# Performance work log

Measured on AMD Instinct MI355X. Metric: run time of the kernel, lower is better.

## Reference

```python
import jax, jax.numpy as jnp
import numpy as np

B = 32; D = 192; DEPTH = 4; DI = 384; DS = 16; DC = 4; P = 16; IMG = 224; N = 196; NC = 2


def setup_inputs() -> dict:
    key = jax.random.key(0)
    ks = iter(jax.random.split(key, 20))
    rn = lambda shape, s=0.02: jax.random.normal(next(ks), shape, dtype=jnp.float32) * s
    inp = {}
    inp["x"] = jax.random.normal(next(ks), (B, 3, IMG, IMG), dtype=jnp.float32)
    inp["patch_w"] = rn((D, 3 * P * P)); inp["patch_b"] = jnp.zeros((D,), jnp.float32)
    inp["cls_token"] = rn((1, 1, D)); inp["pos_embed"] = rn((1, N + 1, D))
    inp["ln_g"] = jnp.ones((DEPTH, D), jnp.float32); inp["ln_b"] = jnp.zeros((DEPTH, D), jnp.float32)
    inp["w_in"] = rn((DEPTH, 2 * DI, D))
    inp["conv_w"] = rn((DEPTH, DI, DC)); inp["conv_b"] = jnp.zeros((DEPTH, DI), jnp.float32)
    inp["w_x"] = rn((DEPTH, 2 * DS + 1, DI))
    inp["w_dt"] = rn((DEPTH, DI)); inp["b_dt"] = jnp.zeros((DEPTH, DI), jnp.float32)
    A = jnp.tile(jnp.arange(1, DS + 1, dtype=jnp.float32)[None, None, :], (DEPTH, DI, 1))
    inp["A_log"] = jnp.log(A)
    inp["D_ssm"] = jnp.ones((DEPTH, DI), jnp.float32)
    inp["w_out"] = rn((DEPTH, D, DI))
    inp["fn_g"] = jnp.ones((D,), jnp.float32); inp["fn_b"] = jnp.zeros((D,), jnp.float32)
    inp["cls_w"] = rn((NC, D)); inp["cls_b"] = jnp.zeros((NC,), jnp.float32)
    inp["reg_w1"] = rn((D // 2, D)); inp["reg_b1"] = jnp.zeros((D // 2,), jnp.float32)
    inp["reg_w2"] = rn((1, D // 2)); inp["reg_b2"] = jnp.zeros((1,), jnp.float32)
    return inp


def _ln(x, g, b):
    m = x.mean(-1, keepdims=True)
    v = ((x - m) ** 2).mean(-1, keepdims=True)
    return (x - m) / jnp.sqrt(v + 1e-5) * g + b


def _mamba(x, w_in, conv_w, conv_b, w_x, w_dt, b_dt, A_log, D_ssm, w_out):
    Bb, L, _ = x.shape
    xz = jnp.einsum('bld,ed->ble', x, w_in)           # [B,L,2*DI]
    xc, z = xz[..., :DI], xz[..., DI:]
    # causal depthwise conv1d (torch pads both sides then slices [:L] -> left-pad DC-1)
    xct = jnp.transpose(xc, (0, 2, 1))                 # [B,DI,L]
    xpad = jnp.pad(xct, ((0, 0), (0, 0), (DC - 1, 0)))
    conv = sum(conv_w[:, k, None] * xpad[:, :, k:k + L] for k in range(DC)) + conv_b[:, None]
    xa = jax.nn.silu(jnp.transpose(conv, (0, 2, 1)))   # [B,L,DI]
    bcd = jnp.einsum('bld,nd->bln', xa, w_x)           # [B,L,2*DS+1]
    Bm = bcd[..., :DS]; Cm = bcd[..., DS:2 * DS]
    dt = jax.nn.softplus(bcd[..., -1:] * w_dt + b_dt)  # [B,L,DI]  (Linear(1,DI))
    A = -jnp.exp(A_log)                                # [DI,DS]
    dA = jnp.exp(dt[..., None] * A)                    # [B,L,DI,DS]
    dBx = dt[..., None] * Bm[:, :, None, :] * xa[..., None]

    def step(h, inp):
        dA_t, dBx_t, C_t = inp
        h = dA_t * h + dBx_t
        return h, jnp.einsum('bdn,bn->bd', h, C_t)

    h0 = jnp.zeros((Bb, DI, DS), dtype=x.dtype)
    _, ys = jax.lax.scan(step, h0, (dA.transpose(1, 0, 2, 3), dBx.transpose(1, 0, 2, 3), Cm.transpose(1, 0, 2)))
    y = jnp.transpose(ys, (1, 0, 2)) + xa * D_ssm
    return jnp.einsum('bli,di->bld', y * jax.nn.silu(z), w_out)


def reference(x, patch_w, patch_b, cls_token, pos_embed, ln_g, ln_b, w_in, conv_w, conv_b,
              w_x, w_dt, b_dt, A_log, D_ssm, w_out, fn_g, fn_b, cls_w, cls_b,
              reg_w1, reg_b1, reg_w2, reg_b2):
    Bb = x.shape[0]
    H = IMG // P
    # non-overlapping patchify == Conv2d(kernel=stride=P)
    patches = x.reshape(Bb, 3, H, P, H, P).transpose(0, 2, 4, 1, 3, 5).reshape(Bb, N, 3 * P * P)
    tok = patches @ patch_w.T + patch_b
    t = jnp.concatenate([jnp.broadcast_to(cls_token, (Bb, 1, D)), tok], axis=1) + pos_embed
    for i in range(DEPTH):
        t = t + _mamba(_ln(t, ln_g[i], ln_b[i]), w_in[i], conv_w[i], conv_b[i],
                       w_x[i], w_dt[i], b_dt[i], A_log[i], D_ssm[i], w_out[i])
    feat = _ln(t, fn_g, fn_b)[:, 0]
    cls = feat @ cls_w.T + cls_b
    reg = jax.nn.gelu(feat @ reg_w1.T + reg_b1, approximate=False) @ reg_w2.T + reg_b2
    return (cls, reg)
```

## Files before the change

kernel.cpp:

```cpp
#include <hip/hip_runtime.h>
#include <hip/hip_bf16.h>
#include <math.h>

#define B_ 32
#define D_ 192
#define DEPTH_ 4
#define DI_ 384
#define DS_ 16
#define DC_ 4
#define P_ 16
#define IMG_ 224
#define N_ 196
#define L_ 197

#define NCH 16
#define CHL 13

typedef short s16x8 __attribute__((ext_vector_type(8)));
typedef float f32x16 __attribute__((ext_vector_type(16)));

__device__ __forceinline__ float sigmoidf_(float x) { return 1.f / (1.f + expf(-x)); }

__global__ __launch_bounds__(256) void k_prep(const float* __restrict__ patch_w,
                                              const float* __restrict__ w_in,
                                              const float* __restrict__ w_out,
                                              const float* __restrict__ w_x,
                                              const float* __restrict__ cls_tok,
                                              const float* __restrict__ pos,
                                              const float* __restrict__ A_log,
                                              __hip_bfloat16* __restrict__ pw,
                                              __hip_bfloat16* __restrict__ win,
                                              __hip_bfloat16* __restrict__ wout,
                                              __hip_bfloat16* __restrict__ wx,
                                              float* __restrict__ t,
                                              float* __restrict__ Aneg) {
  int idx = blockIdx.x * 256 + threadIdx.x;
  if (idx < 147456) { pw[idx] = __float2bfloat16(patch_w[idx]); return; }
  idx -= 147456;
  if (idx < 589824) { win[idx] = __float2bfloat16(w_in[idx]); return; }
  idx -= 589824;
  if (idx < 294912) { wout[idx] = __float2bfloat16(w_out[idx]); return; }
  idx -= 294912;
  if (idx < 98304) {
    int li = idx / 24576;
    int r = (idx / 384) & 63;
    int c = idx % 384;
    wx[idx] = (r < 33) ? __float2bfloat16(w_x[(li * 33 + r) * 384 + c]) : __float2bfloat16(0.f);
    return;
  }
  idx -= 98304;
  if (idx < 6144) {
    int b = idx / 192, d = idx % 192;
    t[(size_t)b * L_ * D_ + d] = cls_tok[d] + pos[d];
    return;
  }
  idx -= 6144;
  Aneg[idx] = -expf(A_log[idx]);
}

__global__ __launch_bounds__(256) void k_im2col(const float* __restrict__ x,
                                                __hip_bfloat16* __restrict__ A) {
  int idx = blockIdx.x * 256 + threadIdx.x;
  int tok = idx / 768, f = idx - tok * 768;
  int b = tok / 196, p = tok - b * 196;
  int h = p / 14, w = p - h * 14;
  int c = f >> 8, i = (f >> 4) & 15, j = f & 15;
  float v = x[(((size_t)(b * 3 + c) * 224 + h * 16 + i) * 224 + w * 16 + j)];
  A[idx] = __float2bfloat16(v);
}

template <int KTOT, int MODE>
__global__ __launch_bounds__(256) void k_gemm_mfma(const short* __restrict__ A,
                                                   const short* __restrict__ Wb,
                                                   float* __restrict__ C,
                                                   const float* __restrict__ bias,
                                                   const float* __restrict__ pos,
                                                   int M) {
  constexpr int KC = 96;
  constexpr int STR = 104;
  __shared__ __align__(16) short Als[64 * STR];
  __shared__ __align__(16) short Bls[64 * STR];
  int m0 = blockIdx.x * 64, n0 = blockIdx.y * 64;
  int tid = threadIdx.x;
  int lane = tid & 63, wid = tid >> 6;
  int mw = (wid & 1) * 32, nw = (wid >> 1) * 32;
  int l31 = lane & 31, lh = lane >> 5;
  f32x16 acc;
#pragma unroll
  for (int i = 0; i < 16; i++) acc[i] = 0.f;
  for (int kc = 0; kc < KTOT; kc += KC) {
    __syncthreads();
#pragma unroll
    for (int i = 0; i < 3; i++) {
      int seg = tid + i * 256;
      int r = seg / 12, s = seg - r * 12;
      *(s16x8*)(Als + r * STR + s * 8) =
          *(const s16x8*)(A + (size_t)(m0 + r) * KTOT + kc + s * 8);
      *(s16x8*)(Bls + r * STR + s * 8) =
          *(const s16x8*)(Wb + (size_t)(n0 + r) * KTOT + kc + s * 8);
    }
    __syncthreads();
#pragma unroll
    for (int ks = 0; ks < KC / 16; ks++) {
      s16x8 af = *(const s16x8*)(Als + (mw + l31) * STR + ks * 16 + lh * 8);
      s16x8 bf = *(const s16x8*)(Bls + (nw + l31) * STR + ks * 16 + lh * 8);
      acc = __builtin_amdgcn_mfma_f32_32x32x16_bf16(af, bf, acc, 0, 0, 0);
    }
  }
  int gn = n0 + nw + l31;
#pragma unroll
  for (int i = 0; i < 16; i++) {
    int rowt = mw + (i & 3) + 8 * (i >> 2) + 4 * lh;
    int gm = m0 + rowt;
    float v = acc[i];
    if (MODE == 1) {
      if (gm < M) C[(size_t)gm * 192 + gn] += v;
    } else if (MODE == 3) {
      if (gm < M) C[(size_t)gm * 64 + gn] = v;
    } else if (MODE == 4) {
      if (gm < M) ((__hip_bfloat16*)C)[(size_t)gm * 768 + gn] = __float2bfloat16(v);
    } else {
      int b = gm / 196, p = gm - b * 196;
      C[((size_t)b * 197 + 1 + p) * 192 + gn] =
          v + bias[gn] + pos[(size_t)(1 + p) * 192 + gn];
    }
  }
}

__global__ __launch_bounds__(256) void k_ln_bf(const float* __restrict__ t,
                                               const float* __restrict__ g,
                                               const float* __restrict__ bb,
                                               __hip_bfloat16* __restrict__ o) {
  int tok = blockIdx.x * 4 + (threadIdx.x >> 6);
  int tid = threadIdx.x & 63;
  const float* xr = t + (size_t)tok * D_;
  float x0 = xr[tid], x1 = xr[tid + 64], x2 = xr[tid + 128];
  float s = x0 + x1 + x2;
  float q = x0 * x0 + x1 * x1 + x2 * x2;
#pragma unroll
  for (int off = 1; off < 64; off <<= 1) {
    s += __shfl_xor(s, off, 64);
    q += __shfl_xor(q, off, 64);
  }
  float m = s * (1.f / 192.f);
  float r = rsqrtf(q * (1.f / 192.f) - m * m + 1e-5f);
  __hip_bfloat16* orow = o + (size_t)tok * D_;
  orow[tid]       = __float2bfloat16((x0 - m) * r * g[tid]       + bb[tid]);
  orow[tid + 64]  = __float2bfloat16((x1 - m) * r * g[tid + 64]  + bb[tid + 64]);
  orow[tid + 128] = __float2bfloat16((x2 - m) * r * g[tid + 128] + bb[tid + 128]);
}

__global__ __launch_bounds__(384) void k_conv(const __hip_bfloat16* __restrict__ xz,
                                              const float* __restrict__ cw_,
                                              const float* __restrict__ cb,
                                              __hip_bfloat16* __restrict__ xa_bf,
                                              __hip_bfloat16* __restrict__ sz_bf) {
  __shared__ float xs[11][384];
  int r0 = blockIdx.x * 8;
  int d = threadIdx.x;
#pragma unroll
  for (int row = 0; row < 11; row++) {
    int gr = r0 - 3 + row;
    if (gr >= 0) xs[row][d] = __bfloat162float(xz[(size_t)gr * 768 + d]);
  }
  __syncthreads();
  float4 cw = *(const float4*)(cw_ + d * 4);
  float cbv = cb[d];
#pragma unroll
  for (int tk = 0; tk < 8; tk++) {
    int tok = r0 + tk;
    int l = tok % L_;
    float acc = fmaf(cw.w, xs[tk + 3][d], cbv);
    if (l >= 1) acc = fmaf(cw.z, xs[tk + 2][d], acc);
    if (l >= 2) acc = fmaf(cw.y, xs[tk + 1][d], acc);
    if (l >= 3) acc = fmaf(cw.x, xs[tk][d], acc);
    float xav = acc * sigmoidf_(acc);
    xa_bf[(size_t)tok * DI_ + d] = __float2bfloat16(xav);
    float z = __bfloat162float(xz[(size_t)tok * 768 + 384 + d]);
    sz_bf[(size_t)tok * DI_ + d] = __float2bfloat16(z * sigmoidf_(z));
  }
}

__global__ __launch_bounds__(384) void k_scan1(const __hip_bfloat16* __restrict__ xa,
                                               const float* __restrict__ bcd,
                                               const float* __restrict__ Aneg,
                                               const float* __restrict__ w_dt,
                                               const float* __restrict__ b_dt,
                                               float* __restrict__ Pst,
                                               float* __restrict__ Hst) {
  int b = blockIdx.x >> 4, ch = blockIdx.x & 15;
  int d = threadIdx.x;
  int l0 = ch * CHL;
  int lim = min(CHL, L_ - l0);
  float Av[16];
#pragma unroll
  for (int q = 0; q < 4; q++) {
    float4 v = *(const float4*)(Aneg + d * 16 + q * 4);
    Av[q * 4] = v.x; Av[q * 4 + 1] = v.y; Av[q * 4 + 2] = v.z; Av[q * 4 + 3] = v.w;
  }
  float wdt = w_dt[d], bdt = b_dt[d];
  const __hip_bfloat16* xap = xa + ((size_t)b * L_ + l0) * DI_ + d;
  const float* bp = bcd + ((size_t)b * L_ + l0) * 64;
  float h[16], Pp[16];
#pragma unroll
  for (int n = 0; n < 16; n++) { h[n] = 0.f; Pp[n] = 1.f; }
  float xv = __bfloat162float(xap[0]);
  for (int j = 0; j < lim; j++) {
    int jn = (j + 1 < lim) ? (j + 1) : j;
    float xn = __bfloat162float(xap[(size_t)jn * DI_]);
    float dtraw = bp[j * 64 + 32];
    float Bn[16];
#pragma unroll
    for (int n = 0; n < 16; n++) Bn[n] = bp[j * 64 + n];
    float v = fmaf(dtraw, wdt, bdt);
    float dtv = (v > 20.f) ? v : __logf(1.f + __expf(v));
    float dtx = dtv * xv;
#pragma unroll
    for (int n = 0; n < 16; n++) {
      float dA = __expf(dtv * Av[n]);
      h[n] = fmaf(dA, h[n], dtx * Bn[n]);
      Pp[n] *= dA;
    }
    xv = xn;
  }
  size_t s = ((size_t)blockIdx.x * 384 + d) * 16;
#pragma unroll
  for (int q = 0; q < 4; q++) {
    *(float4*)(Pst + s + q * 4) = make_float4(Pp[q * 4], Pp[q * 4 + 1], Pp[q * 4 + 2], Pp[q * 4 + 3]);
    *(float4*)(Hst + s + q * 4) = make_float4(h[q * 4], h[q * 4 + 1], h[q * 4 + 2], h[q * 4 + 3]);
  }
}

__global__ __launch_bounds__(256) void k_scan_mid(const float* __restrict__ Pst,
                                                  const float* __restrict__ Hst,
                                                  float* __restrict__ Hinit) {
  int idx = blockIdx.x * 256 + threadIdx.x;
  int b = idx / 6144, r = idx - b * 6144;
  float h = 0.f;
#pragma unroll
  for (int c = 0; c < NCH; c++) {
    size_t o = (size_t)(b * NCH + c) * 6144 + r;
    Hinit[o] = h;
    h = fmaf(Pst[o], h, Hst[o]);
  }
}

__global__ __launch_bounds__(384) void k_scan2(const __hip_bfloat16* __restrict__ xa,
                                               const __hip_bfloat16* __restrict__ sz,
                                               const float* __restrict__ bcd,
                                               const float* __restrict__ Aneg,
                                               const float* __restrict__ D_ssm,
                                               const float* __restrict__ w_dt,
                                               const float* __restrict__ b_dt,
                                               const float* __restrict__ Hinit,
                                               __hip_bfloat16* __restrict__ y) {
  int b = blockIdx.x >> 4, ch = blockIdx.x & 15;
  int d = threadIdx.x;
  int l0 = ch * CHL;
  int lim = min(CHL, L_ - l0);
  float Av[16];
#pragma unroll
  for (int q = 0; q < 4; q++) {
    float4 v = *(const float4*)(Aneg + d * 16 + q * 4);
    Av[q * 4] = v.x; Av[q * 4 + 1] = v.y; Av[q * 4 + 2] = v.z; Av[q * 4 + 3] = v.w;
  }
  float Dv = D_ssm[d];
  float wdt = w_dt[d], bdt = b_dt[d];
  const __hip_bfloat16* xap = xa + ((size_t)b * L_ + l0) * DI_ + d;
  const __hip_bfloat16* szp = sz + ((size_t)b * L_ + l0) * DI_ + d;
  const float* bp = bcd + ((size_t)b * L_ + l0) * 64;
  __hip_bfloat16* yp = y + ((size_t)b * L_ + l0) * DI_ + d;
  float h[16];
  {
    size_t s = ((size_t)blockIdx.x * 384 + d) * 16;
#pragma unroll
    for (int q = 0; q < 4; q++) {
      float4 v = *(const float4*)(Hinit + s + q * 4);
      h[q * 4] = v.x; h[q * 4 + 1] = v.y; h[q * 4 + 2] = v.z; h[q * 4 + 3] = v.w;
    }
  }
  float xv = __bfloat162float(xap[0]);
  float szv = __bfloat162float(szp[0]);
  for (int j = 0; j < lim; j++) {
    int jn = (j + 1 < lim) ? (j + 1) : j;
    float xn = __bfloat162float(xap[(size_t)jn * DI_]);
    float szn = __bfloat162float(szp[(size_t)jn * DI_]);
    float dtraw = bp[j * 64 + 32];
    float Bn[16], Cn[16];
#pragma unroll
    for (int n = 0; n < 16; n++) Bn[n] = bp[j * 64 + n];
#pragma unroll
    for (int n = 0; n < 16; n++) Cn[n] = bp[j * 64 + 16 + n];
    float v = fmaf(dtraw, wdt, bdt);
    float dtv = (v > 20.f) ? v : __logf(1.f + __expf(v));
    float dtx = dtv * xv;
    float acc = 0.f;
#pragma unroll
    for (int n = 0; n < 16; n++) {
      float dA = __expf(dtv * Av[n]);
      h[n] = fmaf(dA, h[n], dtx * Bn[n]);
      acc = fmaf(h[n], Cn[n], acc);
    }
    float yv = fmaf(xv, Dv, acc) * szv;
    yp[(size_t)j * DI_] = __float2bfloat16(yv);
    xv = xn; szv = szn;
  }
}

__global__ __launch_bounds__(192) void k_head(const float* __restrict__ t,
                                              const float* __restrict__ fn_g,
                                              const float* __restrict__ fn_b,
                                              const float* __restrict__ cls_w,
                                              const float* __restrict__ cls_b,
                                              const float* __restrict__ rw1,
                                              const float* __restrict__ rb1,
                                              const float* __restrict__ rw2,
                                              const float* __restrict__ rb2,
                                              float* __restrict__ out) {
  __shared__ float red[8];
  __shared__ float stats[2];
  __shared__ float feat_s[192];
  __shared__ float h_s[96];
  int b = blockIdx.x, tid = threadIdx.x;
  float x = t[(size_t)b * L_ * D_ + tid];
  float s = x, q = x * x;
#pragma unroll
  for (int off = 1; off < 64; off <<= 1) {
    s += __shfl_xor(s, off, 64);
    q += __shfl_xor(q, off, 64);
  }
  int w = tid >> 6;
  if ((tid & 63) == 0) { red[w] = s; red[4 + w] = q; }
  __syncthreads();
  if (tid == 0) {
    float ss = red[0] + red[1] + red[2];
    float qq = red[4] + red[5] + red[6];
    float m = ss * (1.f / 192.f);
    stats[0] = m;
    stats[1] = rsqrtf(qq * (1.f / 192.f) - m * m + 1e-5f);
  }
  __syncthreads();
  float fv = (x - stats[0]) * stats[1] * fn_g[tid] + fn_b[tid];
  feat_s[tid] = fv;
  __syncthreads();
  if (tid < 96) {
    float a = rb1[tid];
    const float* wr = rw1 + (size_t)tid * 192;
    for (int k = 0; k < 192; k++) a = fmaf(feat_s[k], wr[k], a);
    h_s[tid] = 0.5f * a * (1.f + erff(a * 0.70710678118654752f));
  } else if (tid < 98) {
    int c = tid - 96;
    float a = cls_b[c];
    const float* wr = cls_w + (size_t)c * 192;
    for (int k = 0; k < 192; k++) a = fmaf(feat_s[k], wr[k], a);
    out[b * 2 + c] = a;
  }
  __syncthreads();
  if (tid == 0) {
    float a = rb2[0];
    for (int j = 0; j < 96; j++) a = fmaf(h_s[j], rw2[j], a);
    out[64 + b] = a;
  }
}

extern "C" void kernel_launch(void* const* d_in, const int* in_sizes, int n_in,
                              void* d_out, int out_size, void* d_ws, size_t ws_size,
                              hipStream_t stream) {
  const float* x       = (const float*)d_in[0];
  const float* patch_w = (const float*)d_in[1];
  const float* patch_b = (const float*)d_in[2];
  const float* cls_tok = (const float*)d_in[3];
  const float* pos     = (const float*)d_in[4];
  const float* ln_g    = (const float*)d_in[5];
  const float* ln_b    = (const float*)d_in[6];
  const float* w_in    = (const float*)d_in[7];
  const float* conv_w  = (const float*)d_in[8];
  const float* conv_b  = (const float*)d_in[9];
  const float* w_x     = (const float*)d_in[10];
  const float* w_dt    = (const float*)d_in[11];
  const float* b_dt    = (const float*)d_in[12];
  const float* A_log   = (const float*)d_in[13];
  const float* D_ssm   = (const float*)d_in[14];
  const float* w_out   = (const float*)d_in[15];
  const float* fn_g    = (const float*)d_in[16];
  const float* fn_b    = (const float*)d_in[17];
  const float* cls_w   = (const float*)d_in[18];
  const float* cls_b   = (const float*)d_in[19];
  const float* reg_w1  = (const float*)d_in[20];
  const float* reg_b1  = (const float*)d_in[21];
  const float* reg_w2  = (const float*)d_in[22];
  const float* reg_b2  = (const float*)d_in[23];
  float* out = (float*)d_out;

  float* ws = (float*)d_ws;
  float* t_buf = ws;
  float* bcd   = t_buf + 1210368;
  float* Pst   = bcd + 405504;
  float* Hst   = Pst + 3145728;
  float* Hinit = Hst + 3145728;
  float* Aneg  = Hinit + 3145728;
  __hip_bfloat16* xz_bf  = (__hip_bfloat16*)(Aneg + 24576);
  __hip_bfloat16* Abuf   = xz_bf;
  __hip_bfloat16* xa_bf  = xz_bf + 4841472;
  __hip_bfloat16* sz_bf  = xa_bf + 2433024;
  __hip_bfloat16* xln_bf = sz_bf + 2433024;
  __hip_bfloat16* y_bf   = xln_bf + 1216512;
  __hip_bfloat16* pw_bf  = y_bf + 2433024;
  __hip_bfloat16* win_bf = pw_bf + 147456;
  __hip_bfloat16* wout_bf = win_bf + 589824;
  __hip_bfloat16* wx_bf  = wout_bf + 294912;

  k_prep<<<4536, 256, 0, stream>>>(patch_w, w_in, w_out, w_x, cls_tok, pos, A_log,
                                   pw_bf, win_bf, wout_bf, wx_bf, t_buf, Aneg);
  k_im2col<<<18816, 256, 0, stream>>>(x, Abuf);
  k_gemm_mfma<768, 2><<<dim3(98, 3), 256, 0, stream>>>(
      (const short*)Abuf, (const short*)pw_bf, t_buf, patch_b, pos, 6272);

  for (int i = 0; i < DEPTH_; i++) {
    k_ln_bf<<<1576, 256, 0, stream>>>(t_buf, ln_g + i * D_, ln_b + i * D_, xln_bf);
    k_gemm_mfma<192, 4><<<dim3(99, 12), 256, 0, stream>>>(
        (const short*)xln_bf, (const short*)(win_bf + (size_t)i * 147456), (float*)xz_bf,
        nullptr, nullptr, 6304);
    k_conv<<<788, 384, 0, stream>>>(xz_bf, conv_w + i * DI_ * DC_, conv_b + i * DI_,
                                    xa_bf, sz_bf);
    k_gemm_mfma<384, 3><<<dim3(99, 1), 256, 0, stream>>>(
        (const short*)xa_bf, (const short*)(wx_bf + (size_t)i * 24576), bcd,
        nullptr, nullptr, 6304);
    k_scan1<<<B_ * NCH, 384, 0, stream>>>(xa_bf, bcd, Aneg + i * 6144,
                                          w_dt + i * DI_, b_dt + i * DI_, Pst, Hst);
    k_scan_mid<<<768, 256, 0, stream>>>(Pst, Hst, Hinit);
    k_scan2<<<B_ * NCH, 384, 0, stream>>>(xa_bf, sz_bf, bcd, Aneg + i * 6144,
                                          D_ssm + i * DI_, w_dt + i * DI_, b_dt + i * DI_,
                                          Hinit, y_bf);
    k_gemm_mfma<384, 1><<<dim3(99, 3), 256, 0, stream>>>(
        (const short*)y_bf, (const short*)(wout_bf + (size_t)i * 73728), t_buf,
        nullptr, nullptr, 6304);
  }
  k_head<<<32, 192, 0, stream>>>(t_buf, fn_g, fn_b, cls_w, cls_b, reg_w1, reg_b1,
                                 reg_w2, reg_b2, out);
}
```

Before: 462.0 us.

## Fuse LayerNorm into in-projection GEMM, fold scan carry into scan2, merge prep

LayerNorm is now computed inside the in-projection GEMM prologue, so the normalized bf16 activations never go through global memory and one launch per layer is removed. The separate inter-chunk scan kernel is dropped, and each scan2 block instead serially combines the preceding chunks' P/H states itself. The weight-prep and im2col kernels are merged into one launch. The cost is redundant work: LN is recomputed for every N tile (12x), and later chunks in scan2 read up to 15 chunk states each.

```diff
diff --git a/kernel.cpp b/kernel.cpp
--- a/kernel.cpp
+++ b/kernel.cpp
@@ -17,24 +17,35 @@
 #define CHL 13
 
 typedef short s16x8 __attribute__((ext_vector_type(8)));
+typedef short s16x4 __attribute__((ext_vector_type(4)));
 typedef float f32x16 __attribute__((ext_vector_type(16)));
 
 __device__ __forceinline__ float sigmoidf_(float x) { return 1.f / (1.f + expf(-x)); }
-
-__global__ __launch_bounds__(256) void k_prep(const float* __restrict__ patch_w,
-                                              const float* __restrict__ w_in,
-                                              const float* __restrict__ w_out,
-                                              const float* __restrict__ w_x,
-                                              const float* __restrict__ cls_tok,
-                                              const float* __restrict__ pos,
-                                              const float* __restrict__ A_log,
-                                              __hip_bfloat16* __restrict__ pw,
-                                              __hip_bfloat16* __restrict__ win,
-                                              __hip_bfloat16* __restrict__ wout,
-                                              __hip_bfloat16* __restrict__ wx,
-                                              float* __restrict__ t,
-                                              float* __restrict__ Aneg) {
-  int idx = blockIdx.x * 256 + threadIdx.x;
+__device__ __forceinline__ short f2bf(float f) {
+  __hip_bfloat16 h = __float2bfloat16(f);
+  return *(short*)&h;
+}
+
+__global__ __launch_bounds__(256) void k_prep_im2col(
+    const float* __restrict__ x, __hip_bfloat16* __restrict__ A,
+    const float* __restrict__ patch_w, const float* __restrict__ w_in,
+    const float* __restrict__ w_out, const float* __restrict__ w_x,
+    const float* __restrict__ cls_tok, const float* __restrict__ pos,
+    const float* __restrict__ A_log,
+    __hip_bfloat16* __restrict__ pw, __hip_bfloat16* __restrict__ win,
+    __hip_bfloat16* __restrict__ wout, __hip_bfloat16* __restrict__ wx,
+    float* __restrict__ t, float* __restrict__ Aneg) {
+  if (blockIdx.x < 18816) {
+    int idx = blockIdx.x * 256 + threadIdx.x;
+    int tok = idx / 768, f = idx - tok * 768;
+    int b = tok / 196, p = tok - b * 196;
+    int h = p / 14, w = p - h * 14;
+    int c = f >> 8, i = (f >> 4) & 15, j = f & 15;
+    float v = x[(((size_t)(b * 3 + c) * 224 + h * 16 + i) * 224 + w * 16 + j)];
+    A[idx] = __float2bfloat16(v);
+    return;
+  }
+  int idx = (blockIdx.x - 18816) * 256 + threadIdx.x;
   if (idx < 147456) { pw[idx] = __float2bfloat16(patch_w[idx]); return; }
   idx -= 147456;
   if (idx < 589824) { win[idx] = __float2bfloat16(w_in[idx]); return; }
@@ -56,17 +67,6 @@
   }
   idx -= 6144;
   Aneg[idx] = -expf(A_log[idx]);
-}
-
-__global__ __launch_bounds__(256) void k_im2col(const float* __restrict__ x,
-                                                __hip_bfloat16* __restrict__ A) {
-  int idx = blockIdx.x * 256 + threadIdx.x;
-  int tok = idx / 768, f = idx - tok * 768;
-  int b = tok / 196, p = tok - b * 196;
-  int h = p / 14, w = p - h * 14;
-  int c = f >> 8, i = (f >> 4) & 15, j = f & 15;
-  float v = x[(((size_t)(b * 3 + c) * 224 + h * 16 + i) * 224 + w * 16 + j)];
-  A[idx] = __float2bfloat16(v);
 }
 
 template <int KTOT, int MODE>
@@ -113,12 +113,8 @@
     int rowt = mw + (i & 3) + 8 * (i >> 2) + 4 * lh;
     int gm = m0 + rowt;
     float v = acc[i];
-    if (MODE == 1) {
-      if (gm < M) C[(size_t)gm * 192 + gn] += v;
-    } else if (MODE == 3) {
+    if (MODE == 3) {
       if (gm < M) C[(size_t)gm * 64 + gn] = v;
-    } else if (MODE == 4) {
-      if (gm < M) ((__hip_bfloat16*)C)[(size_t)gm * 768 + gn] = __float2bfloat16(v);
     } else {
       int b = gm / 196, p = gm - b * 196;
       C[((size_t)b * 197 + 1 + p) * 192 + gn] =
@@ -127,27 +123,112 @@
   }
 }
 
-__global__ __launch_bounds__(256) void k_ln_bf(const float* __restrict__ t,
-                                               const float* __restrict__ g,
-                                               const float* __restrict__ bb,
-                                               __hip_bfloat16* __restrict__ o) {
-  int tok = blockIdx.x * 4 + (threadIdx.x >> 6);
-  int tid = threadIdx.x & 63;
-  const float* xr = t + (size_t)tok * D_;
-  float x0 = xr[tid], x1 = xr[tid + 64], x2 = xr[tid + 128];
-  float s = x0 + x1 + x2;
-  float q = x0 * x0 + x1 * x1 + x2 * x2;
-#pragma unroll
-  for (int off = 1; off < 64; off <<= 1) {
-    s += __shfl_xor(s, off, 64);
-    q += __shfl_xor(q, off, 64);
-  }
-  float m = s * (1.f / 192.f);
-  float r = rsqrtf(q * (1.f / 192.f) - m * m + 1e-5f);
-  __hip_bfloat16* orow = o + (size_t)tok * D_;
-  orow[tid]       = __float2bfloat16((x0 - m) * r * g[tid]       + bb[tid]);
-  orow[tid + 64]  = __float2bfloat16((x1 - m) * r * g[tid + 64]  + bb[tid + 64]);
-  orow[tid + 128] = __float2bfloat16((x2 - m) * r * g[tid + 128] + bb[tid + 128]);
+__global__ __launch_bounds__(256) void k_gemm_in_ln(const float* __restrict__ t,
+                                                    const float* __restrict__ g,
+                                                    const float* __restrict__ bb,
+                                                    const short* __restrict__ Wb,
+                                                    __hip_bfloat16* __restrict__ xz) {
+  __shared__ __align__(16) short Als[64 * 200];
+  __shared__ __align__(16) short Bls[64 * 200];
+  int m0 = blockIdx.x * 64, n0 = blockIdx.y * 64;
+  int tid = threadIdx.x;
+#pragma unroll
+  for (int i = 0; i < 6; i++) {
+    int seg = tid + i * 256;
+    int r = seg / 24, s = seg - r * 24;
+    *(s16x8*)(Bls + r * 200 + s * 8) =
+        *(const s16x8*)(Wb + (size_t)(n0 + r) * 192 + s * 8);
+  }
+  {
+    int r = tid >> 2, part = tid & 3;
+    int tok = m0 + r;
+    int tokc = (tok < 6304) ? tok : 6303;
+    const float* trow = t + (size_t)tokc * 192 + part * 48;
+    float4 v[12];
+    float s = 0.f, q = 0.f;
+#pragma unroll
+    for (int i = 0; i < 12; i++) {
+      v[i] = *(const float4*)(trow + i * 4);
+      s += v[i].x + v[i].y + v[i].z + v[i].w;
+      q += v[i].x * v[i].x + v[i].y * v[i].y + v[i].z * v[i].z + v[i].w * v[i].w;
+    }
+    s += __shfl_xor(s, 1, 4); s += __shfl_xor(s, 2, 4);
+    q += __shfl_xor(q, 1, 4); q += __shfl_xor(q, 2, 4);
+    float m = s * (1.f / 192.f);
+    float rinv = rsqrtf(q * (1.f / 192.f) - m * m + 1e-5f);
+#pragma unroll
+    for (int i = 0; i < 12; i++) {
+      int c0 = part * 48 + i * 4;
+      s16x4 o;
+      o[0] = f2bf((v[i].x - m) * rinv * g[c0]     + bb[c0]);
+      o[1] = f2bf((v[i].y - m) * rinv * g[c0 + 1] + bb[c0 + 1]);
+      o[2] = f2bf((v[i].z - m) * rinv * g[c0 + 2] + bb[c0 + 2]);
+      o[3] = f2bf((v[i].w - m) * rinv * g[c0 + 3] + bb[c0 + 3]);
+      *(s16x4*)(Als + r * 200 + c0) = o;
+    }
+  }
+  __syncthreads();
+  int lane = tid & 63, wid = tid >> 6;
+  int mw = (wid & 1) * 32, nw = (wid >> 1) * 32;
+  int l31 = lane & 31, lh = lane >> 5;
+  f32x16 acc;
+#pragma unroll
+  for (int i = 0; i < 16; i++) acc[i] = 0.f;
+#pragma unroll
+  for (int ks = 0; ks < 12; ks++) {
+    s16x8 af = *(const s16x8*)(Als + (mw + l31) * 200 + ks * 16 + lh * 8);
+    s16x8 bf = *(const s16x8*)(Bls + (nw + l31) * 200 + ks * 16 + lh * 8);
+    acc = __builtin_amdgcn_mfma_f32_32x32x16_bf16(af, bf, acc, 0, 0, 0);
+  }
+  int gn = n0 + nw + l31;
+#pragma unroll
+  for (int i = 0; i < 16; i++) {
+    int rowt = mw + (i & 3) + 8 * (i >> 2) + 4 * lh;
+    int gm = m0 + rowt;
+    if (gm < 6304) xz[(size_t)gm * 768 + gn] = __float2bfloat16(acc[i]);
+  }
+}
+
+__global__ __launch_bounds__(256) void k_gemm_out(const short* __restrict__ A,
+                                                  const short* __restrict__ Wb,
+                                                  float* __restrict__ C) {
+  constexpr int STR = 104;
+  __shared__ __align__(16) short Als[64 * STR];
+  __shared__ __align__(16) short Bls[64 * STR];
+  int m0 = blockIdx.x * 64, n0 = blockIdx.y * 64;
+  int tid = threadIdx.x;
+  int lane = tid & 63, wid = tid >> 6;
+  int mw = (wid & 1) * 32, nw = (wid >> 1) * 32;
+  int l31 = lane & 31, lh = lane >> 5;
+  f32x16 acc;
+#pragma unroll
+  for (int i = 0; i < 16; i++) acc[i] = 0.f;
+  for (int kc = 0; kc < 384; kc += 96) {
+    __syncthreads();
+#pragma unroll
+    for (int i = 0; i < 3; i++) {
+      int seg = tid + i * 256;
+      int r = seg / 12, s = seg - r * 12;
+      *(s16x8*)(Als + r * STR + s * 8) =
+          *(const s16x8*)(A + (size_t)(m0 + r) * 384 + kc + s * 8);
+      *(s16x8*)(Bls + r * STR + s * 8) =
+          *(const s16x8*)(Wb + (size_t)(n0 + r) * 384 + kc + s * 8);
+    }
+    __syncthreads();
+#pragma unroll
+    for (int ks = 0; ks < 6; ks++) {
+      s16x8 af = *(const s16x8*)(Als + (mw + l31) * STR + ks * 16 + lh * 8);
+      s16x8 bf = *(const s16x8*)(Bls + (nw + l31) * STR + ks * 16 + lh * 8);
+      acc = __builtin_amdgcn_mfma_f32_32x32x16_bf16(af, bf, acc, 0, 0, 0);
+    }
+  }
+  int gn = n0 + nw + l31;
+#pragma unroll
+  for (int i = 0; i < 16; i++) {
+    int rowt = mw + (i & 3) + 8 * (i >> 2) + 4 * lh;
+    int gm = m0 + rowt;
+    if (gm < 6304) C[(size_t)gm * 192 + gn] += acc[i];
+  }
 }
 
 __global__ __launch_bounds__(384) void k_conv(const __hip_bfloat16* __restrict__ xz,
@@ -231,20 +312,6 @@
   }
 }
 
-__global__ __launch_bounds__(256) void k_scan_mid(const float* __restrict__ Pst,
-                                                  const float* __restrict__ Hst,
-                                                  float* __restrict__ Hinit) {
-  int idx = blockIdx.x * 256 + threadIdx.x;
-  int b = idx / 6144, r = idx - b * 6144;
-  float h = 0.f;
-#pragma unroll
-  for (int c = 0; c < NCH; c++) {
-    size_t o = (size_t)(b * NCH + c) * 6144 + r;
-    Hinit[o] = h;
-    h = fmaf(Pst[o], h, Hst[o]);
-  }
-}
-
 __global__ __launch_bounds__(384) void k_scan2(const __hip_bfloat16* __restrict__ xa,
                                                const __hip_bfloat16* __restrict__ sz,
                                                const float* __restrict__ bcd,
@@ -252,7 +319,8 @@
                                                const float* __restrict__ D_ssm,
                                                const float* __restrict__ w_dt,
                                                const float* __restrict__ b_dt,
-                                               const float* __restrict__ Hinit,
+                                               const float* __restrict__ Pst,
+                                               const float* __restrict__ Hst,
                                                __hip_bfloat16* __restrict__ y) {
   int b = blockIdx.x >> 4, ch = blockIdx.x & 15;
   int d = threadIdx.x;
@@ -266,19 +334,25 @@
   }
   float Dv = D_ssm[d];
   float wdt = w_dt[d], bdt = b_dt[d];
+  float h[16];
+#pragma unroll
+  for (int n = 0; n < 16; n++) h[n] = 0.f;
+  for (int c = 0; c < ch; c++) {
+    size_t o = ((size_t)(b * NCH + c) * 384 + d) * 16;
+#pragma unroll
+    for (int q = 0; q < 4; q++) {
+      float4 P = *(const float4*)(Pst + o + q * 4);
+      float4 H = *(const float4*)(Hst + o + q * 4);
+      h[q * 4]     = fmaf(P.x, h[q * 4],     H.x);
+      h[q * 4 + 1] = fmaf(P.y, h[q * 4 + 1], H.y);
+      h[q * 4 + 2] = fmaf(P.z, h[q * 4 + 2], H.z);
+      h[q * 4 + 3] = fmaf(P.w, h[q * 4 + 3], H.w);
+    }
+  }
   const __hip_bfloat16* xap = xa + ((size_t)b * L_ + l0) * DI_ + d;
   const __hip_bfloat16* szp = sz + ((size_t)b * L_ + l0) * DI_ + d;
   const float* bp = bcd + ((size_t)b * L_ + l0) * 64;
   __hip_bfloat16* yp = y + ((size_t)b * L_ + l0) * DI_ + d;
-  float h[16];
-  {
-    size_t s = ((size_t)blockIdx.x * 384 + d) * 16;
-#pragma unroll
-    for (int q = 0; q < 4; q++) {
-      float4 v = *(const float4*)(Hinit + s + q * 4);
-      h[q * 4] = v.x; h[q * 4 + 1] = v.y; h[q * 4 + 2] = v.z; h[q * 4 + 3] = v.w;
-    }
-  }
   float xv = __bfloat162float(xap[0]);
   float szv = __bfloat162float(szp[0]);
   for (int j = 0; j < lim; j++) {
@@ -397,30 +471,27 @@
   float* bcd   = t_buf + 1210368;
   float* Pst   = bcd + 405504;
   float* Hst   = Pst + 3145728;
-  float* Hinit = Hst + 3145728;
-  float* Aneg  = Hinit + 3145728;
+  float* Aneg  = Hst + 3145728;
   __hip_bfloat16* xz_bf  = (__hip_bfloat16*)(Aneg + 24576);
   __hip_bfloat16* Abuf   = xz_bf;
   __hip_bfloat16* xa_bf  = xz_bf + 4841472;
   __hip_bfloat16* sz_bf  = xa_bf + 2433024;
-  __hip_bfloat16* xln_bf = sz_bf + 2433024;
-  __hip_bfloat16* y_bf   = xln_bf + 1216512;
+  __hip_bfloat16* y_bf   = sz_bf + 2433024;
   __hip_bfloat16* pw_bf  = y_bf + 2433024;
   __hip_bfloat16* win_bf = pw_bf + 147456;
   __hip_bfloat16* wout_bf = win_bf + 589824;
   __hip_bfloat16* wx_bf  = wout_bf + 294912;
 
-  k_prep<<<4536, 256, 0, stream>>>(patch_w, w_in, w_out, w_x, cls_tok, pos, A_log,
-                                   pw_bf, win_bf, wout_bf, wx_bf, t_buf, Aneg);
-  k_im2col<<<18816, 256, 0, stream>>>(x, Abuf);
+  k_prep_im2col<<<23352, 256, 0, stream>>>(x, Abuf, patch_w, w_in, w_out, w_x,
+                                           cls_tok, pos, A_log, pw_bf, win_bf,
+                                           wout_bf, wx_bf, t_buf, Aneg);
   k_gemm_mfma<768, 2><<<dim3(98, 3), 256, 0, stream>>>(
       (const short*)Abuf, (const short*)pw_bf, t_buf, patch_b, pos, 6272);
 
   for (int i = 0; i < DEPTH_; i++) {
-    k_ln_bf<<<1576, 256, 0, stream>>>(t_buf, ln_g + i * D_, ln_b + i * D_, xln_bf);
-    k_gemm_mfma<192, 4><<<dim3(99, 12), 256, 0, stream>>>(
-        (const short*)xln_bf, (const short*)(win_bf + (size_t)i * 147456), (float*)xz_bf,
-        nullptr, nullptr, 6304);
+    k_gemm_in_ln<<<dim3(99, 12), 256, 0, stream>>>(
+        t_buf, ln_g + i * D_, ln_b + i * D_,
+        (const short*)(win_bf + (size_t)i * 147456), xz_bf);
     k_conv<<<788, 384, 0, stream>>>(xz_bf, conv_w + i * DI_ * DC_, conv_b + i * DI_,
                                     xa_bf, sz_bf);
     k_gemm_mfma<384, 3><<<dim3(99, 1), 256, 0, stream>>>(
@@ -428,13 +499,11 @@
         nullptr, nullptr, 6304);
     k_scan1<<<B_ * NCH, 384, 0, stream>>>(xa_bf, bcd, Aneg + i * 6144,
                                           w_dt + i * DI_, b_dt + i * DI_, Pst, Hst);
-    k_scan_mid<<<768, 256, 0, stream>>>(Pst, Hst, Hinit);
     k_scan2<<<B_ * NCH, 384, 0, stream>>>(xa_bf, sz_bf, bcd, Aneg + i * 6144,
                                           D_ssm + i * DI_, w_dt + i * DI_, b_dt + i * DI_,
-                                          Hinit, y_bf);
-    k_gemm_mfma<384, 1><<<dim3(99, 3), 256, 0, stream>>>(
-        (const short*)y_bf, (const short*)(wout_bf + (size_t)i * 73728), t_buf,
-        nullptr, nullptr, 6304);
+                                          Pst, Hst, y_bf);
+    k_gemm_out<<<dim3(99, 3), 256, 0, stream>>>(
+        (const short*)y_bf, (const short*)(wout_bf + (size_t)i * 73728), t_buf);
   }
   k_head<<<32, 192, 0, stream>>>(t_buf, fn_g, fn_b, cls_w, cls_b, reg_w1, reg_b1,
                                  reg_w2, reg_b2, out);
```

Result: slower. 564.8 us (+22.2%).

## Fold scan carry propagation into scan2 and merge prep with im2col

Applied to the files above, without the earlier changes.

Removes the k_scan_mid kernel. Each k_scan2 block now rebuilds its starting state by chaining the per-chunk (P, H) summaries of all earlier chunks. This also drops the Hinit buffer and its write/read traffic. The weight prep and im2col kernels are merged into a single launch, so the program has fewer kernel launches and dependency gaps (four fewer per forward from the scan alone). In exchange, later chunks redo up to 15 chunk combines each, which adds redundant global loads to scan2.

```diff
diff --git a/kernel.cpp b/kernel.cpp
--- a/kernel.cpp
+++ b/kernel.cpp
@@ -21,20 +21,26 @@
 
 __device__ __forceinline__ float sigmoidf_(float x) { return 1.f / (1.f + expf(-x)); }
 
-__global__ __launch_bounds__(256) void k_prep(const float* __restrict__ patch_w,
-                                              const float* __restrict__ w_in,
-                                              const float* __restrict__ w_out,
-                                              const float* __restrict__ w_x,
-                                              const float* __restrict__ cls_tok,
-                                              const float* __restrict__ pos,
-                                              const float* __restrict__ A_log,
-                                              __hip_bfloat16* __restrict__ pw,
-                                              __hip_bfloat16* __restrict__ win,
-                                              __hip_bfloat16* __restrict__ wout,
-                                              __hip_bfloat16* __restrict__ wx,
-                                              float* __restrict__ t,
-                                              float* __restrict__ Aneg) {
-  int idx = blockIdx.x * 256 + threadIdx.x;
+__global__ __launch_bounds__(256) void k_prep_im2col(
+    const float* __restrict__ x, __hip_bfloat16* __restrict__ A,
+    const float* __restrict__ patch_w, const float* __restrict__ w_in,
+    const float* __restrict__ w_out, const float* __restrict__ w_x,
+    const float* __restrict__ cls_tok, const float* __restrict__ pos,
+    const float* __restrict__ A_log,
+    __hip_bfloat16* __restrict__ pw, __hip_bfloat16* __restrict__ win,
+    __hip_bfloat16* __restrict__ wout, __hip_bfloat16* __restrict__ wx,
+    float* __restrict__ t, float* __restrict__ Aneg) {
+  if (blockIdx.x < 18816) {
+    int idx = blockIdx.x * 256 + threadIdx.x;
+    int tok = idx / 768, f = idx - tok * 768;
+    int b = tok / 196, p = tok - b * 196;
+    int h = p / 14, w = p - h * 14;
+    int c = f >> 8, i = (f >> 4) & 15, j = f & 15;
+    float v = x[(((size_t)(b * 3 + c) * 224 + h * 16 + i) * 224 + w * 16 + j)];
+    A[idx] = __float2bfloat16(v);
+    return;
+  }
+  int idx = (blockIdx.x - 18816) * 256 + threadIdx.x;
   if (idx < 147456) { pw[idx] = __float2bfloat16(patch_w[idx]); return; }
   idx -= 147456;
   if (idx < 589824) { win[idx] = __float2bfloat16(w_in[idx]); return; }
@@ -56,17 +62,6 @@
   }
   idx -= 6144;
   Aneg[idx] = -expf(A_log[idx]);
-}
-
-__global__ __launch_bounds__(256) void k_im2col(const float* __restrict__ x,
-                                                __hip_bfloat16* __restrict__ A) {
-  int idx = blockIdx.x * 256 + threadIdx.x;
-  int tok = idx / 768, f = idx - tok * 768;
-  int b = tok / 196, p = tok - b * 196;
-  int h = p / 14, w = p - h * 14;
-  int c = f >> 8, i = (f >> 4) & 15, j = f & 15;
-  float v = x[(((size_t)(b * 3 + c) * 224 + h * 16 + i) * 224 + w * 16 + j)];
-  A[idx] = __float2bfloat16(v);
 }
 
 template <int KTOT, int MODE>
@@ -231,20 +226,6 @@
   }
 }
 
-__global__ __launch_bounds__(256) void k_scan_mid(const float* __restrict__ Pst,
-                                                  const float* __restrict__ Hst,
-                                                  float* __restrict__ Hinit) {
-  int idx = blockIdx.x * 256 + threadIdx.x;
-  int b = idx / 6144, r = idx - b * 6144;
-  float h = 0.f;
-#pragma unroll
-  for (int c = 0; c < NCH; c++) {
-    size_t o = (size_t)(b * NCH + c) * 6144 + r;
-    Hinit[o] = h;
-    h = fmaf(Pst[o], h, Hst[o]);
-  }
-}
-
 __global__ __launch_bounds__(384) void k_scan2(const __hip_bfloat16* __restrict__ xa,
                                                const __hip_bfloat16* __restrict__ sz,
                                                const float* __restrict__ bcd,
@@ -252,7 +233,8 @@
                                                const float* __restrict__ D_ssm,
                                                const float* __restrict__ w_dt,
                                                const float* __restrict__ b_dt,
-                                               const float* __restrict__ Hinit,
+                                               const float* __restrict__ Pst,
+                                               const float* __restrict__ Hst,
                                                __hip_bfloat16* __restrict__ y) {
   int b = blockIdx.x >> 4, ch = blockIdx.x & 15;
   int d = threadIdx.x;
@@ -266,19 +248,25 @@
   }
   float Dv = D_ssm[d];
   float wdt = w_dt[d], bdt = b_dt[d];
+  float h[16];
+#pragma unroll
+  for (int n = 0; n < 16; n++) h[n] = 0.f;
+  for (int c = 0; c < ch; c++) {
+    size_t o = ((size_t)(b * NCH + c) * 384 + d) * 16;
+#pragma unroll
+    for (int q = 0; q < 4; q++) {
+      float4 P = *(const float4*)(Pst + o + q * 4);
+      float4 H = *(const float4*)(Hst + o + q * 4);
+      h[q * 4]     = fmaf(P.x, h[q * 4],     H.x);
+      h[q * 4 + 1] = fmaf(P.y, h[q * 4 + 1], H.y);
+      h[q * 4 + 2] = fmaf(P.z, h[q * 4 + 2], H.z);
+      h[q * 4 + 3] = fmaf(P.w, h[q * 4 + 3], H.w);
+    }
+  }
   const __hip_bfloat16* xap = xa + ((size_t)b * L_ + l0) * DI_ + d;
   const __hip_bfloat16* szp = sz + ((size_t)b * L_ + l0) * DI_ + d;
   const float* bp = bcd + ((size_t)b * L_ + l0) * 64;
   __hip_bfloat16* yp = y + ((size_t)b * L_ + l0) * DI_ + d;
-  float h[16];
-  {
-    size_t s = ((size_t)blockIdx.x * 384 + d) * 16;
-#pragma unroll
-    for (int q = 0; q < 4; q++) {
-      float4 v = *(const float4*)(Hinit + s + q * 4);
-      h[q * 4] = v.x; h[q * 4 + 1] = v.y; h[q * 4 + 2] = v.z; h[q * 4 + 3] = v.w;
-    }
-  }
   float xv = __bfloat162float(xap[0]);
   float szv = __bfloat162float(szp[0]);
   for (int j = 0; j < lim; j++) {
@@ -397,8 +385,7 @@
   float* bcd   = t_buf + 1210368;
   float* Pst   = bcd + 405504;
   float* Hst   = Pst + 3145728;
-  float* Hinit = Hst + 3145728;
-  float* Aneg  = Hinit + 3145728;
+  float* Aneg  = Hst + 3145728;
   __hip_bfloat16* xz_bf  = (__hip_bfloat16*)(Aneg + 24576);
   __hip_bfloat16* Abuf   = xz_bf;
   __hip_bfloat16* xa_bf  = xz_bf + 4841472;
@@ -410,9 +397,9 @@
   __hip_bfloat16* wout_bf = win_bf + 589824;
   __hip_bfloat16* wx_bf  = wout_bf + 294912;
 
-  k_prep<<<4536, 256, 0, stream>>>(patch_w, w_in, w_out, w_x, cls_tok, pos, A_log,
-                                   pw_bf, win_bf, wout_bf, wx_bf, t_buf, Aneg);
-  k_im2col<<<18816, 256, 0, stream>>>(x, Abuf);
+  k_prep_im2col<<<23352, 256, 0, stream>>>(x, Abuf, patch_w, w_in, w_out, w_x,
+                                           cls_tok, pos, A_log, pw_bf, win_bf,
+                                           wout_bf, wx_bf, t_buf, Aneg);
   k_gemm_mfma<768, 2><<<dim3(98, 3), 256, 0, stream>>>(
       (const short*)Abuf, (const short*)pw_bf, t_buf, patch_b, pos, 6272);
 
@@ -428,10 +415,9 @@
         nullptr, nullptr, 6304);
     k_scan1<<<B_ * NCH, 384, 0, stream>>>(xa_bf, bcd, Aneg + i * 6144,
                                           w_dt + i * DI_, b_dt + i * DI_, Pst, Hst);
-    k_scan_mid<<<768, 256, 0, stream>>>(Pst, Hst, Hinit);
     k_scan2<<<B_ * NCH, 384, 0, stream>>>(xa_bf, sz_bf, bcd, Aneg + i * 6144,
                                           D_ssm + i * DI_, w_dt + i * DI_, b_dt + i * DI_,
-                                          Hinit, y_bf);
+                                          Pst, Hst, y_bf);
     k_gemm_mfma<384, 1><<<dim3(99, 3), 256, 0, stream>>>(
         (const short*)y_bf, (const short*)(wout_bf + (size_t)i * 73728), t_buf,
         nullptr, nullptr, 6304);
```

Result: slower. 536.3 us (+16.1%).
